# Kernel tuning notes

Measured on AMD Instinct MI355X. Metric: run time of the kernel, lower is better.

The kernel has to match this reference:

```python
import jax, jax.numpy as jnp
import numpy as np

BETA = 0.9
THRESH = 1.0
SLOPE = 25.0  # snntorch fast_sigmoid default slope
T = 4096

@jax.custom_vjp
def spike_fn(x):
    # Heaviside forward, fast-sigmoid surrogate backward
    return (x > 0).astype(x.dtype)

def _spike_fwd(x):
    return (x > 0).astype(x.dtype), x

def _spike_bwd(x, g):
    return (g / (SLOPE * jnp.abs(x) + 1.0) ** 2,)

spike_fn.defvjp(_spike_fwd, _spike_bwd)

def setup_inputs():
    key = jax.random.key(0)
    ks = jax.random.split(key, 5)
    B = 1024
    x = jax.random.normal(ks[0], (B, 6, T), dtype=jnp.float32)
    W1 = jax.random.normal(ks[1], (10, 6), dtype=jnp.float32) / np.sqrt(6.0)
    b1 = jax.random.normal(ks[2], (10,), dtype=jnp.float32) * 0.01
    W2 = jax.random.normal(ks[3], (27, 10), dtype=jnp.float32) / np.sqrt(10.0)
    b2 = jax.random.normal(ks[4], (27,), dtype=jnp.float32) * 0.01
    return {"x": x, "W1": W1, "b1": b1, "W2": W2, "b2": b2}

def reference(x, W1, b1, W2, b2):
    B = x.shape[0]
    xt = jnp.transpose(x, (2, 0, 1))  # [T, B, 6]
    mem1_0 = jnp.zeros((B, 10), x.dtype)
    mem2_0 = jnp.zeros((B, 27), x.dtype)

    def step(carry, xin):
        mem1, mem2 = carry
        cur1 = xin @ W1.T + b1                              # [B,10]
        rst1 = jax.lax.stop_gradient((mem1 > THRESH).astype(x.dtype))
        mem1 = BETA * mem1 + cur1 - rst1 * THRESH           # subtract reset
        spk1 = spike_fn(mem1 - THRESH)
        cur2 = spk1 @ W2.T + b2                             # [B,27]
        rst2 = jax.lax.stop_gradient((mem2 > THRESH).astype(x.dtype))
        mem2 = BETA * mem2 + cur2 - rst2 * THRESH
        return (mem1, mem2), None

    (mem1, mem2), _ = jax.lax.scan(step, (mem1_0, mem2_0), xt)
    # module returns only the spike of the final timestep
    return spike_fn(mem2 - THRESH)
```

## Files before the change

### kernel.cpp

```cpp
#include <hip/hip_runtime.h>


#define T_STEPS 4096
#define BETA 0.9f
#define THRESH 1.0f
#define CH 64
#define NCHUNK (T_STEPS / CH)

__global__ __launch_bounds__(64, 1) void snn_kernel(
    const float* __restrict__ x,
    const float* __restrict__ W1,
    const float* __restrict__ b1,
    const float* __restrict__ W2,
    const float* __restrict__ b2,
    float* __restrict__ out)
{
    __shared__ float tabLo[32 * 28];
    __shared__ float tabHi[32 * 28];
    __shared__ float curBuf[2][10 * 68];

    const int l = threadIdx.x;
    const int b = blockIdx.x;

    if (l < 32) {
        for (int j = 0; j < 27; ++j) {
            float slo = b2[j];
            float shi = 0.0f;
            #pragma unroll
            for (int i = 0; i < 5; ++i) {
                if (l & (1 << i)) {
                    slo += W2[j * 10 + i];
                    shi += W2[j * 10 + 5 + i];
                }
            }
            tabLo[l * 28 + j] = slo;
            tabHi[l * 28 + j] = shi;
        }
    }

    float w1r[60], b1r[10];
    #pragma unroll
    for (int i = 0; i < 10; ++i) {
        b1r[i] = b1[i];
        #pragma unroll
        for (int c = 0; c < 6; ++c) w1r[i * 6 + c] = W1[i * 6 + c];
    }

    __syncthreads();

    const int ri = (l < 10) ? l : 9;
    const int rj = (l < 27) ? l : 26;

    float mem1 = 0.0f, mem2 = 0.0f;
    float spkf = 0.0f;
    float rstf2 = 0.0f;

    const float* xb = x + (size_t)b * 6 * T_STEPS;

    float xv[6], xn[6];
    #pragma unroll
    for (int c = 0; c < 6; ++c) xv[c] = xb[c * T_STEPS + l];

    for (int k = 0; k < NCHUNK; ++k) {
        const int buf = k & 1;

        if (k + 1 < NCHUNK) {
            #pragma unroll
            for (int c = 0; c < 6; ++c) xn[c] = xb[c * T_STEPS + (k + 1) * CH + l];
        }

        #pragma unroll
        for (int i = 0; i < 10; ++i) {
            float acc = xv[0] * w1r[i * 6 + 0];
            acc = fmaf(xv[1], w1r[i * 6 + 1], acc);
            acc = fmaf(xv[2], w1r[i * 6 + 2], acc);
            acc = fmaf(xv[3], w1r[i * 6 + 3], acc);
            acc = fmaf(xv[4], w1r[i * 6 + 4], acc);
            acc = fmaf(xv[5], w1r[i * 6 + 5], acc);
            curBuf[buf][i * 68 + l] = acc + b1r[i];
        }
        __syncthreads();

        const float* cp = &curBuf[buf][ri * 68];
        #pragma unroll 1
        for (int t8 = 0; t8 < CH; t8 += 8) {
            float4 q0 = *(const float4*)(cp + t8);
            float4 q1 = *(const float4*)(cp + t8 + 4);
            float c1v[8] = {q0.x, q0.y, q0.z, q0.w, q1.x, q1.y, q1.z, q1.w};

            int mlo[8], mhi[8];
            #pragma unroll
            for (int s = 0; s < 8; ++s) {
                float t1 = fmaf(BETA, mem1, c1v[s]);
                mem1 = t1 - spkf;
                bool spk = mem1 > THRESH;
                unsigned long long bal = __ballot(spk);
                spkf = spk ? 1.0f : 0.0f;
                mlo[s] = (int)(bal & 31);
                mhi[s] = (int)((bal >> 5) & 31);
            }
            float tlo[8], thi[8];
            #pragma unroll
            for (int s = 0; s < 8; ++s) {
                tlo[s] = tabLo[mlo[s] * 28 + rj];
                thi[s] = tabHi[mhi[s] * 28 + rj];
            }
            #pragma unroll
            for (int s = 0; s < 8; ++s) {
                float cur2 = tlo[s] + thi[s];
                float t2 = fmaf(BETA, mem2, cur2);
                mem2 = t2 - rstf2;
                rstf2 = (mem2 > THRESH) ? 1.0f : 0.0f;
            }
        }

        #pragma unroll
        for (int c = 0; c < 6; ++c) xv[c] = xn[c];
    }

    if (l < 27) {
        out[b * 27 + l] = (mem2 > THRESH) ? 1.0f : 0.0f;
    }
}

extern "C" void kernel_launch(void* const* d_in, const int* in_sizes, int n_in,
                              void* d_out, int out_size, void* d_ws, size_t ws_size,
                              hipStream_t stream) {
    const float* x  = (const float*)d_in[0];
    const float* W1 = (const float*)d_in[1];
    const float* b1 = (const float*)d_in[2];
    const float* W2 = (const float*)d_in[3];
    const float* b2 = (const float*)d_in[4];
    float* out = (float*)d_out;

    const int B = in_sizes[0] / (6 * T_STEPS);
    snn_kernel<<<dim3(B), dim3(64), 0, stream>>>(x, W1, b1, W2, b2, out);
}
```

Measured before the change: 363.6 us.

## Software-pipeline layer-1 ballots with layer-2 table lookups and drop barriers

Restructures the per-chunk time loop so the next 8-step group's layer-1 membrane updates and ballots run while the current group's layer-2 table lookups and updates are in flight. This hides the LDS lookup latency behind the serial layer-1 chain. It also drops both __syncthreads and the double-buffered cur buffer, since the block is a single wavefront. The spike tables move to a stride of 32 with pre-shifted indices, and reset subtraction becomes a boolean select. Removing the barriers relies on the compiler keeping the order of cross-lane LDS writes and reads inside one wave.

```diff
diff --git a/kernel.cpp b/kernel.cpp
--- a/kernel.cpp
+++ b/kernel.cpp
@@ -6,6 +6,8 @@
 #define THRESH 1.0f
 #define CH 64
 #define NCHUNK (T_STEPS / CH)
+#define GRP 8
+#define NGRP (CH / GRP)
 
 __global__ __launch_bounds__(64, 1) void snn_kernel(
     const float* __restrict__ x,
@@ -15,9 +17,9 @@
     const float* __restrict__ b2,
     float* __restrict__ out)
 {
-    __shared__ float tabLo[32 * 28];
-    __shared__ float tabHi[32 * 28];
-    __shared__ float curBuf[2][10 * 68];
+    __shared__ float tabLo[32 * 32];
+    __shared__ float tabHi[32 * 32];
+    __shared__ float curBuf[10 * 68];
 
     const int l = threadIdx.x;
     const int b = blockIdx.x;
@@ -33,8 +35,8 @@
                     shi += W2[j * 10 + 5 + i];
                 }
             }
-            tabLo[l * 28 + j] = slo;
-            tabHi[l * 28 + j] = shi;
+            tabLo[l * 32 + j] = slo;
+            tabHi[l * 32 + j] = shi;
         }
     }
 
@@ -46,29 +48,22 @@
         for (int c = 0; c < 6; ++c) w1r[i * 6 + c] = W1[i * 6 + c];
     }
 
-    __syncthreads();
-
     const int ri = (l < 10) ? l : 9;
     const int rj = (l < 27) ? l : 26;
 
     float mem1 = 0.0f, mem2 = 0.0f;
-    float spkf = 0.0f;
-    float rstf2 = 0.0f;
+    bool sp1 = false;
+    bool sp2 = false;
 
     const float* xb = x + (size_t)b * 6 * T_STEPS;
-
     float xv[6], xn[6];
     #pragma unroll
     for (int c = 0; c < 6; ++c) xv[c] = xb[c * T_STEPS + l];
 
+    const float* cp = &curBuf[ri * 68];
+
+    #pragma unroll 1
     for (int k = 0; k < NCHUNK; ++k) {
-        const int buf = k & 1;
-
-        if (k + 1 < NCHUNK) {
-            #pragma unroll
-            for (int c = 0; c < 6; ++c) xn[c] = xb[c * T_STEPS + (k + 1) * CH + l];
-        }
-
         #pragma unroll
         for (int i = 0; i < 10; ++i) {
             float acc = xv[0] * w1r[i * 6 + 0];
@@ -77,49 +72,85 @@
             acc = fmaf(xv[3], w1r[i * 6 + 3], acc);
             acc = fmaf(xv[4], w1r[i * 6 + 4], acc);
             acc = fmaf(xv[5], w1r[i * 6 + 5], acc);
-            curBuf[buf][i * 68 + l] = acc + b1r[i];
+            curBuf[i * 68 + l] = acc + b1r[i];
         }
-        __syncthreads();
 
-        const float* cp = &curBuf[buf][ri * 68];
-        #pragma unroll 1
-        for (int t8 = 0; t8 < CH; t8 += 8) {
-            float4 q0 = *(const float4*)(cp + t8);
-            float4 q1 = *(const float4*)(cp + t8 + 4);
+        if (k + 1 < NCHUNK) {
+            #pragma unroll
+            for (int c = 0; c < 6; ++c) xn[c] = xb[c * T_STEPS + (k + 1) * CH + l];
+        }
+
+        unsigned mlo[GRP], mhi[GRP];
+
+        {
+            float4 q0 = *(const float4*)(cp + 0);
+            float4 q1 = *(const float4*)(cp + 4);
             float c1v[8] = {q0.x, q0.y, q0.z, q0.w, q1.x, q1.y, q1.z, q1.w};
-
-            int mlo[8], mhi[8];
             #pragma unroll
             for (int s = 0; s < 8; ++s) {
                 float t1 = fmaf(BETA, mem1, c1v[s]);
-                mem1 = t1 - spkf;
-                bool spk = mem1 > THRESH;
-                unsigned long long bal = __ballot(spk);
-                spkf = spk ? 1.0f : 0.0f;
-                mlo[s] = (int)(bal & 31);
-                mhi[s] = (int)((bal >> 5) & 31);
+                mem1 = sp1 ? (t1 - THRESH) : t1;
+                sp1 = mem1 > THRESH;
+                unsigned m = (unsigned)__ballot(sp1);
+                mlo[s] = (m & 31u) << 5;
+                mhi[s] = ((m >> 5) & 31u) << 5;
             }
+        }
+
+        #pragma unroll
+        for (int g = 0; g < NGRP; ++g) {
+            const bool more = (g + 1 < NGRP);
+
+            float c1n[8];
+            if (more) {
+                float4 p0 = *(const float4*)(cp + (g + 1) * 8);
+                float4 p1 = *(const float4*)(cp + (g + 1) * 8 + 4);
+                c1n[0] = p0.x; c1n[1] = p0.y; c1n[2] = p0.z; c1n[3] = p0.w;
+                c1n[4] = p1.x; c1n[5] = p1.y; c1n[6] = p1.z; c1n[7] = p1.w;
+            }
+
             float tlo[8], thi[8];
             #pragma unroll
             for (int s = 0; s < 8; ++s) {
-                tlo[s] = tabLo[mlo[s] * 28 + rj];
-                thi[s] = tabHi[mhi[s] * 28 + rj];
+                tlo[s] = tabLo[mlo[s] + rj];
+                thi[s] = tabHi[mhi[s] + rj];
             }
+
+            unsigned nlo[GRP], nhi[GRP];
+            if (more) {
+                #pragma unroll
+                for (int s = 0; s < 8; ++s) {
+                    float t1 = fmaf(BETA, mem1, c1n[s]);
+                    mem1 = sp1 ? (t1 - THRESH) : t1;
+                    sp1 = mem1 > THRESH;
+                    unsigned m = (unsigned)__ballot(sp1);
+                    nlo[s] = (m & 31u) << 5;
+                    nhi[s] = ((m >> 5) & 31u) << 5;
+                }
+            }
+
             #pragma unroll
             for (int s = 0; s < 8; ++s) {
                 float cur2 = tlo[s] + thi[s];
                 float t2 = fmaf(BETA, mem2, cur2);
-                mem2 = t2 - rstf2;
-                rstf2 = (mem2 > THRESH) ? 1.0f : 0.0f;
+                mem2 = sp2 ? (t2 - THRESH) : t2;
+                sp2 = mem2 > THRESH;
+            }
+
+            if (more) {
+                #pragma unroll
+                for (int s = 0; s < 8; ++s) { mlo[s] = nlo[s]; mhi[s] = nhi[s]; }
             }
         }
 
-        #pragma unroll
-        for (int c = 0; c < 6; ++c) xv[c] = xn[c];
+        if (k + 1 < NCHUNK) {
+            #pragma unroll
+            for (int c = 0; c < 6; ++c) xv[c] = xn[c];
+        }
     }
 
     if (l < 27) {
-        out[b * 27 + l] = (mem2 > THRESH) ? 1.0f : 0.0f;
+        out[b * 27 + l] = sp2 ? 1.0f : 0.0f;
     }
 }
 
```

Measured after the change: 310.1 us. 1.17x faster.

## Replace LDS spike lookup tables with lane broadcasts and per-lane register FMAs

Applied to the files above, without the earlier changes.

Removes the shared-memory current buffer and the W2 subset-sum lookup tables. Each timestep now broadcasts the six inputs with readlane, computes the layer-1 current per lane, then rebuilds layer-2 current from the ballot mask using ten FMAs against register-held W2 weights. This drops LDS traffic and the per-chunk barrier, but adds about sixteen extra VALU ops and six readlanes per serial timestep, all on the critical dependency chain.

```diff
diff --git a/kernel.cpp b/kernel.cpp
--- a/kernel.cpp
+++ b/kernel.cpp
@@ -7,6 +7,10 @@
 #define CH 64
 #define NCHUNK (T_STEPS / CH)
 
+__device__ __forceinline__ float lane_bcast(float v, int lane) {
+    return __int_as_float(__builtin_amdgcn_readlane(__float_as_int(v), lane));
+}
+
 __global__ __launch_bounds__(64, 1) void snn_kernel(
     const float* __restrict__ x,
     const float* __restrict__ W1,
@@ -15,111 +19,84 @@
     const float* __restrict__ b2,
     float* __restrict__ out)
 {
-    __shared__ float tabLo[32 * 28];
-    __shared__ float tabHi[32 * 28];
-    __shared__ float curBuf[2][10 * 68];
-
     const int l = threadIdx.x;
     const int b = blockIdx.x;
-
-    if (l < 32) {
-        for (int j = 0; j < 27; ++j) {
-            float slo = b2[j];
-            float shi = 0.0f;
-            #pragma unroll
-            for (int i = 0; i < 5; ++i) {
-                if (l & (1 << i)) {
-                    slo += W2[j * 10 + i];
-                    shi += W2[j * 10 + 5 + i];
-                }
-            }
-            tabLo[l * 28 + j] = slo;
-            tabHi[l * 28 + j] = shi;
-        }
-    }
-
-    float w1r[60], b1r[10];
-    #pragma unroll
-    for (int i = 0; i < 10; ++i) {
-        b1r[i] = b1[i];
-        #pragma unroll
-        for (int c = 0; c < 6; ++c) w1r[i * 6 + c] = W1[i * 6 + c];
-    }
-
-    __syncthreads();
 
     const int ri = (l < 10) ? l : 9;
     const int rj = (l < 27) ? l : 26;
 
+    float w1row[6];
+    #pragma unroll
+    for (int c = 0; c < 6; ++c) w1row[c] = W1[ri * 6 + c];
+    const float b1i = b1[ri];
+
+    float w2c[10];
+    #pragma unroll
+    for (int i = 0; i < 10; ++i) w2c[i] = W2[rj * 10 + i];
+    const float b2j = b2[rj];
+
     float mem1 = 0.0f, mem2 = 0.0f;
-    float spkf = 0.0f;
-    float rstf2 = 0.0f;
+    bool  sp1 = false, sp2 = false;
 
     const float* xb = x + (size_t)b * 6 * T_STEPS;
-
     float xv[6], xn[6];
     #pragma unroll
     for (int c = 0; c < 6; ++c) xv[c] = xb[c * T_STEPS + l];
 
+    #pragma unroll 1
     for (int k = 0; k < NCHUNK; ++k) {
-        const int buf = k & 1;
-
         if (k + 1 < NCHUNK) {
             #pragma unroll
             for (int c = 0; c < 6; ++c) xn[c] = xb[c * T_STEPS + (k + 1) * CH + l];
         }
 
         #pragma unroll
-        for (int i = 0; i < 10; ++i) {
-            float acc = xv[0] * w1r[i * 6 + 0];
-            acc = fmaf(xv[1], w1r[i * 6 + 1], acc);
-            acc = fmaf(xv[2], w1r[i * 6 + 2], acc);
-            acc = fmaf(xv[3], w1r[i * 6 + 3], acc);
-            acc = fmaf(xv[4], w1r[i * 6 + 4], acc);
-            acc = fmaf(xv[5], w1r[i * 6 + 5], acc);
-            curBuf[buf][i * 68 + l] = acc + b1r[i];
-        }
-        __syncthreads();
+        for (int s = 0; s < CH; ++s) {
+            const float x0 = lane_bcast(xv[0], s);
+            const float x1 = lane_bcast(xv[1], s);
+            const float x2 = lane_bcast(xv[2], s);
+            const float x3 = lane_bcast(xv[3], s);
+            const float x4 = lane_bcast(xv[4], s);
+            const float x5 = lane_bcast(xv[5], s);
 
-        const float* cp = &curBuf[buf][ri * 68];
-        #pragma unroll 1
-        for (int t8 = 0; t8 < CH; t8 += 8) {
-            float4 q0 = *(const float4*)(cp + t8);
-            float4 q1 = *(const float4*)(cp + t8 + 4);
-            float c1v[8] = {q0.x, q0.y, q0.z, q0.w, q1.x, q1.y, q1.z, q1.w};
+            float acc = x0 * w1row[0];
+            acc = fmaf(x1, w1row[1], acc);
+            acc = fmaf(x2, w1row[2], acc);
+            acc = fmaf(x3, w1row[3], acc);
+            acc = fmaf(x4, w1row[4], acc);
+            acc = fmaf(x5, w1row[5], acc);
+            const float c1 = acc + b1i;
 
-            int mlo[8], mhi[8];
-            #pragma unroll
-            for (int s = 0; s < 8; ++s) {
-                float t1 = fmaf(BETA, mem1, c1v[s]);
-                mem1 = t1 - spkf;
-                bool spk = mem1 > THRESH;
-                unsigned long long bal = __ballot(spk);
-                spkf = spk ? 1.0f : 0.0f;
-                mlo[s] = (int)(bal & 31);
-                mhi[s] = (int)((bal >> 5) & 31);
-            }
-            float tlo[8], thi[8];
-            #pragma unroll
-            for (int s = 0; s < 8; ++s) {
-                tlo[s] = tabLo[mlo[s] * 28 + rj];
-                thi[s] = tabHi[mhi[s] * 28 + rj];
-            }
-            #pragma unroll
-            for (int s = 0; s < 8; ++s) {
-                float cur2 = tlo[s] + thi[s];
-                float t2 = fmaf(BETA, mem2, cur2);
-                mem2 = t2 - rstf2;
-                rstf2 = (mem2 > THRESH) ? 1.0f : 0.0f;
-            }
+            float t1 = fmaf(BETA, mem1, c1);
+            mem1 = sp1 ? (t1 - THRESH) : t1;
+            sp1 = mem1 > THRESH;
+
+            const unsigned m = (unsigned)__ballot(sp1) & 0x3FFu;
+
+            float cur2 = fmaf((m & 1u)         ? 1.0f : 0.0f, w2c[0], b2j);
+            cur2 = fmaf(((m >> 1) & 1u) ? 1.0f : 0.0f, w2c[1], cur2);
+            cur2 = fmaf(((m >> 2) & 1u) ? 1.0f : 0.0f, w2c[2], cur2);
+            cur2 = fmaf(((m >> 3) & 1u) ? 1.0f : 0.0f, w2c[3], cur2);
+            cur2 = fmaf(((m >> 4) & 1u) ? 1.0f : 0.0f, w2c[4], cur2);
+            cur2 = fmaf(((m >> 5) & 1u) ? 1.0f : 0.0f, w2c[5], cur2);
+            cur2 = fmaf(((m >> 6) & 1u) ? 1.0f : 0.0f, w2c[6], cur2);
+            cur2 = fmaf(((m >> 7) & 1u) ? 1.0f : 0.0f, w2c[7], cur2);
+            cur2 = fmaf(((m >> 8) & 1u) ? 1.0f : 0.0f, w2c[8], cur2);
+            cur2 = fmaf(((m >> 9) & 1u) ? 1.0f : 0.0f, w2c[9], cur2);
+
+            float t2 = fmaf(BETA, mem2, cur2);
+            mem2 = sp2 ? (t2 - THRESH) : t2;
+            sp2 = mem2 > THRESH;
         }
 
-        #pragma unroll
-        for (int c = 0; c < 6; ++c) xv[c] = xn[c];
+        if (k + 1 < NCHUNK) {
+            #pragma unroll
+            for (int c = 0; c < 6; ++c) xv[c] = xn[c];
+        }
     }
 
     if (l < 27) {
-        out[b * 27 + l] = (mem2 > THRESH) ? 1.0f : 0.0f;
+        out[b * 27 + l] = sp2 ? 1.0f : 0.0f;
     }
 }
 
```

Result: slower. 583.4 us (+60.4%).
